# Kernel optimization log

Measured on AMD Instinct MI355X. Metric: run time of the kernel, lower is better.

## Reference

```python
import jax, jax.numpy as jnp
import numpy as np

GS, GL, LS, LL, NA = 8, 8, 16, 8, 12
ALPHA = 0.5


def _rgb_to_lab(img):
    # img: (B,3,H,W) in [0,1]. Standard sRGB -> CIELab (kornia convention).
    lin = jnp.where(img > 0.04045, ((img + 0.055) / 1.055) ** 2.4, img / 12.92)
    r, g, b = lin[:, 0], lin[:, 1], lin[:, 2]
    x = 0.412453 * r + 0.357580 * g + 0.180423 * b
    y = 0.212671 * r + 0.715160 * g + 0.072169 * b
    z = 0.019334 * r + 0.119193 * g + 0.950227 * b
    xn, yn, zn = x / 0.950456, y, z / 1.088754
    f = lambda t: jnp.where(t > 0.008856, jnp.cbrt(t), 7.787 * t + 4.0 / 29.0)
    fx, fy, fz = f(xn), f(yn), f(zn)
    L = 116.0 * fy - 16.0
    a = 500.0 * (fx - fy)
    bb = 200.0 * (fy - fz)
    return L, a, bb


def _bilateral_slice(grid, img, guide):
    # grid: (B,12,s,s,l); img: (B,3,H,W); guide: (B,H,W) in [0,1]
    B, C, s, _, l = grid.shape
    _, _, H, W = img.shape
    g5 = jnp.transpose(grid, (0, 4, 2, 3, 1))  # (B, D=l, Hg=s, Wg=s, C)
    # align_corners=True coordinates, border padding == clamp
    fx = jnp.linspace(0.0, s - 1.0, W)                    # (W,)
    fy = jnp.linspace(0.0, s - 1.0, H)                    # (H,)
    fz = jnp.clip(guide * (l - 1.0), 0.0, l - 1.0)        # (B,H,W)
    x0 = jnp.floor(fx).astype(jnp.int32); x1 = jnp.minimum(x0 + 1, s - 1)
    y0 = jnp.floor(fy).astype(jnp.int32); y1 = jnp.minimum(y0 + 1, s - 1)
    z0 = jnp.floor(fz).astype(jnp.int32); z1 = jnp.minimum(z0 + 1, l - 1)
    wx = (fx - x0)[None, None, :, None]
    wy = (fy - y0)[None, :, None, None]
    wz = (fz - z0)[..., None]
    bi = jnp.arange(B)[:, None, None]
    yi0, yi1 = y0[None, :, None], y1[None, :, None]
    xi0, xi1 = x0[None, None, :], x1[None, None, :]

    def gat(zi, yi, xi):
        return g5[bi, zi, yi, xi]  # (B,H,W,C)

    def bilin(zi):
        c00 = gat(zi, yi0, xi0) * (1 - wx) + gat(zi, yi0, xi1) * wx
        c10 = gat(zi, yi1, xi0) * (1 - wx) + gat(zi, yi1, xi1) * wx
        return c00 * (1 - wy) + c10 * wy

    coeffs = bilin(z0) * (1 - wz) + bilin(z1) * wz       # (B,H,W,12)
    A = coeffs[..., :9].reshape(B, H, W, 3, 3)
    bvec = coeffs[..., 9:]
    img_hwc = jnp.transpose(img, (0, 2, 3, 1))           # (B,H,W,3)
    out = jnp.einsum('bhwck,bhwk->bhwc', A, img_hwc) + bvec
    return jnp.transpose(jnp.clip(out, 0.0, 1.0), (0, 3, 1, 2))


def setup_inputs() -> dict:
    key = jax.random.key(0)
    ks = jax.random.split(key, 16)
    B, H, W = 4, 896, 896
    n_h = n_w = 64
    inp = {
        'R_spatial': jax.random.normal(ks[0], (B, 256, n_h, n_w), jnp.float32),
        'F_sem': jax.random.normal(ks[1], (B, n_h * n_w, 384), jnp.float32),
        'img': jax.random.uniform(ks[2], (B, 3, H, W), jnp.float32),
        'n_h': n_h,
        'n_w': n_w,
    }
    sc = 0.02
    identity = np.array([1., 0., 0., 0., 1., 0., 0., 0., 1., 0., 0., 0.], np.float32)
    inp['dino_proj_w'] = jax.random.normal(ks[3], (128, 384), jnp.float32) * sc
    inp['dino_proj_b'] = jnp.zeros((128,), jnp.float32)
    inp['fusion_w'] = jax.random.normal(ks[4], (256, 384), jnp.float32) * sc
    inp['fusion_b'] = jnp.zeros((256,), jnp.float32)
    inp['g1_w'] = jax.random.normal(ks[5], (256, 256), jnp.float32) * sc
    inp['g1_b'] = jnp.zeros((256,), jnp.float32)
    inp['g2_w'] = jax.random.normal(ks[6], (NA * GS * GS * GL, 256), jnp.float32) * sc
    inp['g2_b'] = jnp.asarray(np.repeat(identity, GS * GS * GL))  # identity init
    inp['local_w'] = jax.random.normal(ks[7], (NA * LL, 256), jnp.float32) * sc
    inp['local_b'] = jnp.asarray(np.repeat(identity, LL))
    inp['guide_w1'] = jax.random.normal(ks[8], (64, 384), jnp.float32) * sc
    inp['guide_b1'] = jnp.zeros((64,), jnp.float32)
    inp['guide_w2'] = jax.random.normal(ks[9], (1, 64), jnp.float32) * sc
    inp['guide_b2'] = jnp.zeros((1,), jnp.float32)
    return inp


def reference(R_spatial, F_sem, img, n_h, n_w,
              dino_proj_w, dino_proj_b, fusion_w, fusion_b,
              g1_w, g1_b, g2_w, g2_b, local_w, local_b,
              guide_w1, guide_b1, guide_w2, guide_b2):
    B, _, H, W = img.shape
    # ---- GridNet ----
    F_sp = jnp.transpose(F_sem, (0, 2, 1)).reshape(B, 384, n_h, n_w)
    proj = jnp.einsum('bchw,oc->bohw', F_sp, dino_proj_w) + dino_proj_b[None, :, None, None]
    fused_in = jnp.concatenate([R_spatial, proj], axis=1)
    fused = jnp.einsum('bchw,oc->bohw', fused_in, fusion_w) + fusion_b[None, :, None, None]
    f_gap = fused.mean(axis=(-2, -1))                       # (B,256)
    h = jax.nn.relu(f_gap @ g1_w.T + g1_b)
    G_global = (h @ g2_w.T + g2_b).reshape(B, NA, GS, GS, GL)
    kh, kw = n_h // LS, n_w // LS
    pooled = fused.reshape(B, 256, LS, kh, LS, kw).mean(axis=(3, 5))
    lflat = jnp.einsum('bchw,oc->bohw', pooled, local_w) + local_b[None, :, None, None]
    G_local = jnp.transpose(lflat.reshape(B, NA, LL, LS, LS), (0, 1, 3, 4, 2))
    # ---- SemanticGuide ----
    L, a, bb = _rgb_to_lab(img)
    g_chroma = jnp.clip((0.5 * L + 0.25 * jnp.abs(a) + 0.25 * jnp.abs(bb)) / 114.0, 0.0, 1.0)
    hsem = jax.nn.relu(jnp.einsum('bnd,hd->bnh', F_sem, guide_w1) + guide_b1)
    g_sem_patch = jax.nn.sigmoid(jnp.einsum('bnh,oh->bno', hsem, guide_w2) + guide_b2)
    g_sem_patch = g_sem_patch.reshape(B, n_h, n_w, 1).transpose(0, 3, 1, 2)
    g_sem = jax.image.resize(g_sem_patch, (B, 1, H, W), 'bilinear')[:, 0]
    g = ALPHA * g_chroma + (1.0 - ALPHA) * g_sem
    # ---- slice + apply ----
    I_global = _bilateral_slice(G_global, img, g)
    I_local = _bilateral_slice(G_local, img, g)
    return I_global, I_local, G_global, G_local, g
```

## Files before the change

### kernel.cpp

```cpp
#include <hip/hip_runtime.h>
#include <math.h>

#define HWPIX 802816
#define OUT_IL 9633792
#define OUT_GG 19267584
#define OUT_GL 19292160
#define OUT_G  19390464

#define WS_WT4  0
#define WS_BC   163840
#define WS_POOL 164096
#define WS_H    426240
#define WS_GSEM 427264
#define WS_RG   443648
#define WS_RL   468224
#define WS_W1T  566528

__device__ __forceinline__ float fast_exp2(float x) {
  return __builtin_amdgcn_exp2f(x);
}
__device__ __forceinline__ float fast_log2(float x) {
  return __builtin_amdgcn_logf(x);
}
__device__ __forceinline__ float srgb_lin(float v) {
  float p = fast_exp2(2.4f * fast_log2((v + 0.055f) * (1.0f / 1.055f)));
  return v > 0.04045f ? p : v * (1.0f / 12.92f);
}
__device__ __forceinline__ float labf(float t) {
  float c = fast_exp2((1.0f / 3.0f) * fast_log2(t));
  return t > 0.008856f ? c : 7.787f * t + (4.0f / 29.0f);
}

__global__ __launch_bounds__(256) void k_prep(
    const float* __restrict__ fus_w, const float* __restrict__ fus_b,
    const float* __restrict__ dino_w, const float* __restrict__ dino_b,
    const float* __restrict__ gw1, float* __restrict__ Wt4,
    float* __restrict__ bc, float* __restrict__ w1T) {
  if (blockIdx.x == 641) {
    int t = threadIdx.x;
    for (int it = 0; it < 96; ++it) {
      int idx = it * 256 + t;
      int h = idx & 63;
      int k = idx >> 6;
      w1T[((k >> 2) * 64 + h) * 4 + (k & 3)] = gw1[h * 384 + k];
    }
    return;
  }
  if (blockIdx.x == 640) {
    int o = threadIdx.x;
    float acc = fus_b[o];
    for (int m = 0; m < 128; ++m) acc += fus_w[o * 384 + 256 + m] * dino_b[m];
    bc[o] = acc;
    return;
  }
  int idx = blockIdx.x * 256 + threadIdx.x;
  int o = idx / 640;
  int k = idx - o * 640;
  float val;
  if (k < 256) {
    val = fus_w[o * 384 + k];
  } else {
    int d = k - 256;
    float acc = 0.0f;
    for (int m = 0; m < 128; ++m)
      acc += fus_w[o * 384 + 256 + m] * dino_w[m * 384 + d];
    val = acc;
  }
  Wt4[((k >> 2) * 256 + o) * 4 + (k & 3)] = val;
}

__global__ __launch_bounds__(1024) void k_fused_pool(
    const float* __restrict__ R, const float* __restrict__ F,
    const float* __restrict__ Wt4, const float* __restrict__ bc,
    float* __restrict__ pooled) {
  int blk = blockIdx.x;
  int b = blk >> 6;
  int i = (blk >> 2) & 15;
  int jg = blk & 3;
  int t = threadIdx.x;
  int cell = t >> 8;
  int c = t & 255;
  __shared__ float s[4 * 640];
  {
    const float* rb = R + (((b * 256 + c) * 64 + i * 4) * 64) + (jg * 4 + cell) * 4;
    float p = 0.0f;
#pragma unroll
    for (int di = 0; di < 4; ++di) {
      float4 v = *(const float4*)(rb + di * 64);
      p += v.x + v.y + v.z + v.w;
    }
    s[cell * 640 + c] = p;
  }
  {
    float a0 = 0.0f, a1 = 0.0f;
    const float* fb = F + (size_t)(b * 4096 + (i * 4) * 64 + (jg * 4 + cell) * 4) * 384;
#pragma unroll
    for (int pix = 0; pix < 16; ++pix) {
      const float* fr = fb + (size_t)((pix >> 2) * 64 + (pix & 3)) * 384;
      a0 += fr[c];
      if (c < 128) a1 += fr[256 + c];
    }
    s[cell * 640 + 256 + c] = a0;
    if (c < 128) s[cell * 640 + 512 + c] = a1;
  }
  __syncthreads();
  float acc = 0.0f;
  const float4* w4 = (const float4*)Wt4;
  const float4* s4 = (const float4*)(s + cell * 640);
#pragma unroll 8
  for (int kk = 0; kk < 160; ++kk) {
    float4 wv = w4[kk * 256 + c];
    float4 sv = s4[kk];
    acc += wv.x * sv.x + wv.y * sv.y + wv.z * sv.z + wv.w * sv.w;
  }
  __syncthreads();
  s[cell * 256 + c] = acc;
  __syncthreads();
  if (t < 256) {
    float bco = bc[t];
    float4 v;
    v.x = s[0 * 256 + t] * (1.0f / 16.0f) + bco;
    v.y = s[1 * 256 + t] * (1.0f / 16.0f) + bco;
    v.z = s[2 * 256 + t] * (1.0f / 16.0f) + bco;
    v.w = s[3 * 256 + t] * (1.0f / 16.0f) + bco;
    *(float4*)(pooled + ((size_t)(b * 256 + t) * 256) + i * 16 + jg * 4) = v;
  }
}

__global__ __launch_bounds__(1024) void k_gap(
    const float* __restrict__ pooled, const float* __restrict__ g1_w,
    const float* __restrict__ g1_b, float* __restrict__ hout) {
  int b = blockIdx.x;
  int t = threadIdx.x;
  int o = t & 255;
  int q = t >> 8;
  __shared__ float f[256];
  __shared__ float part[4][256];
  {
    const float4* pr4 = (const float4*)(pooled + (size_t)(b * 256 + o) * 256 + q * 64);
    float s = 0.0f;
#pragma unroll
    for (int i = 0; i < 16; ++i) {
      float4 v = pr4[i];
      s += v.x + v.y + v.z + v.w;
    }
    part[q][o] = s;
  }
  __syncthreads();
  if (t < 256)
    f[t] = (part[0][t] + part[1][t] + part[2][t] + part[3][t]) * (1.0f / 256.0f);
  __syncthreads();
  {
    const float4* wr = (const float4*)(g1_w + o * 256 + q * 64);
    const float4* fq = (const float4*)(f + q * 64);
    float acc = 0.0f;
#pragma unroll
    for (int i = 0; i < 16; ++i) {
      float4 w = wr[i];
      float4 fv = fq[i];
      acc += w.x * fv.x + w.y * fv.y + w.z * fv.z + w.w * fv.w;
    }
    part[q][o] = acc;
  }
  __syncthreads();
  if (t < 256) {
    float a = part[0][t] + part[1][t] + part[2][t] + part[3][t] + g1_b[t];
    hout[b * 256 + t] = fmaxf(a, 0.0f);
  }
}

__global__ __launch_bounds__(256) void k_gglobal(
    const float* __restrict__ h, const float* __restrict__ g2_w,
    const float* __restrict__ g2_b, float* __restrict__ out3,
    float* __restrict__ rg) {
  int b = blockIdx.x / 24;
  int o = (blockIdx.x % 24) * 256 + threadIdx.x;
  __shared__ float hl[256];
  hl[threadIdx.x] = h[b * 256 + threadIdx.x];
  __syncthreads();
  float acc = g2_b[o];
  const float* wr = g2_w + o * 256;
  for (int k = 0; k < 256; ++k) acc += wr[k] * hl[k];
  out3[b * 6144 + o] = acc;
  int n = o >> 9, y = (o >> 6) & 7, x = (o >> 3) & 7, z = o & 7;
  rg[b * 6144 + ((y * 8 + x) * 8 + z) * 12 + n] = acc;
}

__global__ __launch_bounds__(256) void k_glocal(
    const float* __restrict__ pooled, const float* __restrict__ lw,
    const float* __restrict__ lb, float* __restrict__ out4,
    float* __restrict__ rl) {
  int idx = blockIdx.x * 256 + threadIdx.x;
  int b = idx / 24576;
  int r = idx - b * 24576;
  int o = r >> 8;
  int cell = r & 255;
  float acc = lb[o];
  const float* wr = lw + o * 256;
  const float* pr = pooled + b * 65536 + cell;
  for (int c = 0; c < 256; ++c) acc += wr[c] * pr[c * 256];
  int n = o >> 3, l = o & 7;
  out4[((b * 12 + n) * 256 + cell) * 8 + l] = acc;
  rl[b * 24576 + (cell * 8 + l) * 12 + n] = acc;
}

__global__ __launch_bounds__(256) void k_guide(
    const float* __restrict__ F, const float* __restrict__ w1T,
    const float* __restrict__ b1, const float* __restrict__ w2,
    const float* __restrict__ b2, float* __restrict__ gsem) {
  int t = threadIdx.x;
  int wave = t >> 6;
  int lane = t & 63;
  int pb = blockIdx.x * 16;
  __shared__ float4 sF[16 * 96];
  const float4* Fb = (const float4*)(F + (size_t)pb * 384);
#pragma unroll
  for (int r = 0; r < 6; ++r) sF[r * 256 + t] = Fb[r * 256 + t];
  __syncthreads();
  float accp[4] = {0.0f, 0.0f, 0.0f, 0.0f};
  const float4* w4 = (const float4*)w1T;
  int prow = wave * 4;
  for (int c = 0; c < 48; ++c) {
    float4 wa = w4[(c * 2 + 0) * 64 + lane];
    float4 wb = w4[(c * 2 + 1) * 64 + lane];
#pragma unroll
    for (int p = 0; p < 4; ++p) {
      float4 va = sF[(prow + p) * 96 + c * 2 + 0];
      float4 vb = sF[(prow + p) * 96 + c * 2 + 1];
      accp[p] += va.x * wa.x + va.y * wa.y + va.z * wa.z + va.w * wa.w +
                 vb.x * wb.x + vb.y * wb.y + vb.z * wb.z + vb.w * wb.w;
    }
  }
  float hb = b1[lane];
  float wl = w2[lane];
  float b2v = b2[0];
  float res = 0.0f;
#pragma unroll
  for (int p = 0; p < 4; ++p) {
    float v = fmaxf(accp[p] + hb, 0.0f) * wl;
#pragma unroll
    for (int m = 32; m >= 1; m >>= 1) v += __shfl_xor(v, m, 64);
    if (lane == p) res = v;
  }
  if (lane < 4) gsem[pb + prow + lane] = 1.0f / (1.0f + expf(-(res + b2v)));
}

template <int SDIM>
__device__ __forceinline__ void slice_lds(
    const float* __restrict__ sg, int w, int z0, int z1, float wz,
    float r, float g, float bl, float& o0, float& o1, float& o2) {
  constexpr float sc = (float)(SDIM - 1) * (1.0f / 895.0f);
  float fxs = (float)w * sc;
  int x0 = (int)fxs;
  if (x0 > SDIM - 1) x0 = SDIM - 1;
  int x1 = x0 < SDIM - 1 ? x0 + 1 : SDIM - 1;
  float wx = fxs - (float)x0;
  float wz0 = 1.0f - wz;
  float w00 = (1.0f - wx) * wz0;
  float w01 = (1.0f - wx) * wz;
  float w10 = wx * wz0;
  float w11 = wx * wz;
  const float4* p00 = (const float4*)(sg + (x0 * 8 + z0) * 12);
  const float4* p01 = (const float4*)(sg + (x0 * 8 + z1) * 12);
  const float4* p10 = (const float4*)(sg + (x1 * 8 + z0) * 12);
  const float4* p11 = (const float4*)(sg + (x1 * 8 + z1) * 12);
  float a[12];
#pragma unroll
  for (int c = 0; c < 3; ++c) {
    float4 v00 = p00[c], v01 = p01[c], v10 = p10[c], v11 = p11[c];
    a[4 * c + 0] = w00 * v00.x + w01 * v01.x + w10 * v10.x + w11 * v11.x;
    a[4 * c + 1] = w00 * v00.y + w01 * v01.y + w10 * v10.y + w11 * v11.y;
    a[4 * c + 2] = w00 * v00.z + w01 * v01.z + w10 * v10.z + w11 * v11.z;
    a[4 * c + 3] = w00 * v00.w + w01 * v01.w + w10 * v10.w + w11 * v11.w;
  }
  o0 = fminf(fmaxf(a[0] * r + a[1] * g + a[2] * bl + a[9], 0.0f), 1.0f);
  o1 = fminf(fmaxf(a[3] * r + a[4] * g + a[5] * bl + a[10], 0.0f), 1.0f);
  o2 = fminf(fmaxf(a[6] * r + a[7] * g + a[8] * bl + a[11], 0.0f), 1.0f);
}

__global__ __launch_bounds__(448) void k_pixel(
    const float* __restrict__ img, const float* __restrict__ gsem,
    const float* __restrict__ rg, const float* __restrict__ rl,
    float* __restrict__ out) {
  int blk = blockIdx.x;
  int b = blk / 896;
  int h = blk - b * 896;
  int t = threadIdx.x;
  __shared__ float sgr[64];
  __shared__ float sG[768];
  __shared__ float sL[1536];

  float sy = fminf(fmaxf((h + 0.5f) * (1.0f / 14.0f) - 0.5f, 0.0f), 63.0f);
  int y0s = (int)sy;
  int y1s = y0s < 63 ? y0s + 1 : 63;
  float wys = sy - (float)y0s;
  float fyg = (float)h * (7.0f / 895.0f);
  int y0g = (int)fyg;
  if (y0g > 7) y0g = 7;
  int y1g = y0g < 7 ? y0g + 1 : 7;
  float wyg = fyg - (float)y0g;
  float fyl = (float)h * (15.0f / 895.0f);
  int y0l = (int)fyl;
  if (y0l > 15) y0l = 15;
  int y1l = y0l < 15 ? y0l + 1 : 15;
  float wyl = fyl - (float)y0l;

  if (t < 64) {
    const float* gb = gsem + b * 4096;
    sgr[t] = gb[y0s * 64 + t] * (1.0f - wys) + gb[y1s * 64 + t] * wys;
  }
  {
    const float* g0 = rg + b * 6144 + y0g * 768;
    const float* g1 = rg + b * 6144 + y1g * 768;
    for (int i = t; i < 768; i += 448)
      sG[i] = g0[i] * (1.0f - wyg) + g1[i] * wyg;
    const float* l0 = rl + b * 24576 + y0l * 1536;
    const float* l1 = rl + b * 24576 + y1l * 1536;
    for (int i = t; i < 1536; i += 448)
      sL[i] = l0[i] * (1.0f - wyl) + l1[i] * wyl;
  }
  __syncthreads();

#pragma unroll
  for (int ip = 0; ip < 2; ++ip) {
    int w = ip * 448 + t;
    int hw = h * 896 + w;
    float r = img[(b * 3 + 0) * HWPIX + hw];
    float g = img[(b * 3 + 1) * HWPIX + hw];
    float bl = img[(b * 3 + 2) * HWPIX + hw];
    float lr = srgb_lin(r), lg = srgb_lin(g), lb2 = srgb_lin(bl);
    float X = 0.412453f * lr + 0.357580f * lg + 0.180423f * lb2;
    float Y = 0.212671f * lr + 0.715160f * lg + 0.072169f * lb2;
    float Z = 0.019334f * lr + 0.119193f * lg + 0.950227f * lb2;
    float fx_ = labf(X * (1.0f / 0.950456f));
    float fy_ = labf(Y);
    float fz_ = labf(Z * (1.0f / 1.088754f));
    float gch = 0.50877193f * fy_ - 0.070175439f +
                1.0964912f * fabsf(fx_ - fy_) + 0.43859649f * fabsf(fy_ - fz_);
    gch = fminf(fmaxf(gch, 0.0f), 1.0f);
    float sx = fminf(fmaxf((w + 0.5f) * (1.0f / 14.0f) - 0.5f, 0.0f), 63.0f);
    int x0s = (int)sx;
    int x1s = x0s < 63 ? x0s + 1 : 63;
    float wxs = sx - (float)x0s;
    float gs = sgr[x0s] * (1.0f - wxs) + sgr[x1s] * wxs;
    float gg = 0.5f * gch + 0.5f * gs;
    __builtin_nontemporal_store(gg, &out[OUT_G + b * HWPIX + hw]);
    float fzc = fminf(fmaxf(gg * 7.0f, 0.0f), 7.0f);
    int z0 = (int)fzc;
    if (z0 > 7) z0 = 7;
    int z1 = z0 < 7 ? z0 + 1 : 7;
    float wz = fzc - (float)z0;
    float o0, o1, o2;
    slice_lds<8>(sG, w, z0, z1, wz, r, g, bl, o0, o1, o2);
    __builtin_nontemporal_store(o0, &out[(b * 3 + 0) * HWPIX + hw]);
    __builtin_nontemporal_store(o1, &out[(b * 3 + 1) * HWPIX + hw]);
    __builtin_nontemporal_store(o2, &out[(b * 3 + 2) * HWPIX + hw]);
    slice_lds<16>(sL, w, z0, z1, wz, r, g, bl, o0, o1, o2);
    __builtin_nontemporal_store(o0, &out[OUT_IL + (b * 3 + 0) * HWPIX + hw]);
    __builtin_nontemporal_store(o1, &out[OUT_IL + (b * 3 + 1) * HWPIX + hw]);
    __builtin_nontemporal_store(o2, &out[OUT_IL + (b * 3 + 2) * HWPIX + hw]);
  }
}

extern "C" void kernel_launch(void* const* d_in, const int* in_sizes, int n_in,
                              void* d_out, int out_size, void* d_ws,
                              size_t ws_size, hipStream_t stream) {
  const float* R = (const float*)d_in[0];
  const float* F = (const float*)d_in[1];
  const float* img = (const float*)d_in[2];
  const float* dino_w = (const float*)d_in[5];
  const float* dino_b = (const float*)d_in[6];
  const float* fus_w = (const float*)d_in[7];
  const float* fus_b = (const float*)d_in[8];
  const float* g1_w = (const float*)d_in[9];
  const float* g1_b = (const float*)d_in[10];
  const float* g2_w = (const float*)d_in[11];
  const float* g2_b = (const float*)d_in[12];
  const float* lw = (const float*)d_in[13];
  const float* lb = (const float*)d_in[14];
  const float* gw1 = (const float*)d_in[15];
  const float* gb1 = (const float*)d_in[16];
  const float* gw2 = (const float*)d_in[17];
  const float* gb2 = (const float*)d_in[18];
  float* out = (float*)d_out;
  float* ws = (float*)d_ws;

  float* Wt4 = ws + WS_WT4;
  float* bc = ws + WS_BC;
  float* pooled = ws + WS_POOL;
  float* hbuf = ws + WS_H;
  float* gsem = ws + WS_GSEM;
  float* rg = ws + WS_RG;
  float* rl = ws + WS_RL;
  float* w1T = ws + WS_W1T;

  k_prep<<<642, 256, 0, stream>>>(fus_w, fus_b, dino_w, dino_b, gw1, Wt4, bc, w1T);
  k_guide<<<1024, 256, 0, stream>>>(F, w1T, gb1, gw2, gb2, gsem);
  k_fused_pool<<<256, 1024, 0, stream>>>(R, F, Wt4, bc, pooled);
  k_gap<<<4, 1024, 0, stream>>>(pooled, g1_w, g1_b, hbuf);
  k_gglobal<<<96, 256, 0, stream>>>(hbuf, g2_w, g2_b, out + OUT_GG, rg);
  k_glocal<<<384, 256, 0, stream>>>(pooled, lw, lb, out + OUT_GL, rl);
  k_pixel<<<3584, 448, 0, stream>>>(img, gsem, rg, rl, out);
}
```

Measured before the change: 324.1 us.

## Fuse local grid projection into pooling kernel and split-K the global grid matvec

The local-grid 1x1 projection moves from its own kernel into the tail of k_fused_pool, using the pooled values still held in shared memory and a transposed copy of the local weights built in k_prep. This removes one kernel launch and the strided re-read of the pooled buffer. k_gglobal now splits its 256-long dot product across four thread groups with float4 loads and a shared-memory reduction. The fused tail runs a serial 256-step loop per thread on part of the block, which lengthens the pooling kernel.

```diff
diff --git a/kernel.cpp b/kernel.cpp
--- a/kernel.cpp
+++ b/kernel.cpp
@@ -15,6 +15,7 @@
 #define WS_RG   443648
 #define WS_RL   468224
 #define WS_W1T  566528
+#define WS_LWT  591104
 
 __device__ __forceinline__ float fast_exp2(float x) {
   return __builtin_amdgcn_exp2f(x);
@@ -34,8 +35,19 @@
 __global__ __launch_bounds__(256) void k_prep(
     const float* __restrict__ fus_w, const float* __restrict__ fus_b,
     const float* __restrict__ dino_w, const float* __restrict__ dino_b,
-    const float* __restrict__ gw1, float* __restrict__ Wt4,
-    float* __restrict__ bc, float* __restrict__ w1T) {
+    const float* __restrict__ gw1, const float* __restrict__ lw,
+    float* __restrict__ Wt4, float* __restrict__ bc, float* __restrict__ w1T,
+    float* __restrict__ lwT) {
+  if (blockIdx.x == 642) {
+    int t = threadIdx.x;
+    for (int it = 0; it < 96; ++it) {
+      int idx = it * 256 + t;
+      int o = idx >> 8;
+      int c = idx & 255;
+      lwT[c * 96 + o] = lw[o * 256 + c];
+    }
+    return;
+  }
   if (blockIdx.x == 641) {
     int t = threadIdx.x;
     for (int it = 0; it < 96; ++it) {
@@ -72,7 +84,9 @@
 __global__ __launch_bounds__(1024) void k_fused_pool(
     const float* __restrict__ R, const float* __restrict__ F,
     const float* __restrict__ Wt4, const float* __restrict__ bc,
-    float* __restrict__ pooled) {
+    const float* __restrict__ lwT, const float* __restrict__ lb,
+    float* __restrict__ pooled, float* __restrict__ out4,
+    float* __restrict__ rl) {
   int blk = blockIdx.x;
   int b = blk >> 6;
   int i = (blk >> 2) & 15;
@@ -124,6 +138,20 @@
     v.z = s[2 * 256 + t] * (1.0f / 16.0f) + bco;
     v.w = s[3 * 256 + t] * (1.0f / 16.0f) + bco;
     *(float4*)(pooled + ((size_t)(b * 256 + t) * 256) + i * 16 + jg * 4) = v;
+  } else if (t < 640) {
+    int idx = t - 256;
+    int cl = idx / 96;
+    int o = idx - cl * 96;
+    const float* sc_ = s + cl * 256;
+    float acc2 = lb[o];
+    for (int cc = 0; cc < 256; ++cc) {
+      float pv = sc_[cc] * (1.0f / 16.0f) + bc[cc];
+      acc2 += lwT[cc * 96 + o] * pv;
+    }
+    int cellg = i * 16 + jg * 4 + cl;
+    int n = o >> 3, l = o & 7;
+    out4[((b * 12 + n) * 256 + cellg) * 8 + l] = acc2;
+    rl[b * 24576 + (cellg * 8 + l) * 12 + n] = acc2;
   }
 }
 
@@ -169,39 +197,39 @@
   }
 }
 
-__global__ __launch_bounds__(256) void k_gglobal(
+__global__ __launch_bounds__(1024) void k_gglobal(
     const float* __restrict__ h, const float* __restrict__ g2_w,
     const float* __restrict__ g2_b, float* __restrict__ out3,
     float* __restrict__ rg) {
   int b = blockIdx.x / 24;
-  int o = (blockIdx.x % 24) * 256 + threadIdx.x;
+  int og = (blockIdx.x % 24) * 256;
+  int t = threadIdx.x;
+  int ol = t & 255;
+  int q = t >> 8;
   __shared__ float hl[256];
-  hl[threadIdx.x] = h[b * 256 + threadIdx.x];
-  __syncthreads();
-  float acc = g2_b[o];
-  const float* wr = g2_w + o * 256;
-  for (int k = 0; k < 256; ++k) acc += wr[k] * hl[k];
-  out3[b * 6144 + o] = acc;
-  int n = o >> 9, y = (o >> 6) & 7, x = (o >> 3) & 7, z = o & 7;
-  rg[b * 6144 + ((y * 8 + x) * 8 + z) * 12 + n] = acc;
-}
-
-__global__ __launch_bounds__(256) void k_glocal(
-    const float* __restrict__ pooled, const float* __restrict__ lw,
-    const float* __restrict__ lb, float* __restrict__ out4,
-    float* __restrict__ rl) {
-  int idx = blockIdx.x * 256 + threadIdx.x;
-  int b = idx / 24576;
-  int r = idx - b * 24576;
-  int o = r >> 8;
-  int cell = r & 255;
-  float acc = lb[o];
-  const float* wr = lw + o * 256;
-  const float* pr = pooled + b * 65536 + cell;
-  for (int c = 0; c < 256; ++c) acc += wr[c] * pr[c * 256];
-  int n = o >> 3, l = o & 7;
-  out4[((b * 12 + n) * 256 + cell) * 8 + l] = acc;
-  rl[b * 24576 + (cell * 8 + l) * 12 + n] = acc;
+  __shared__ float part[4][256];
+  if (t < 256) hl[t] = h[b * 256 + t];
+  __syncthreads();
+  {
+    const float4* wr = (const float4*)(g2_w + (size_t)(og + ol) * 256 + q * 64);
+    const float4* hq = (const float4*)(hl + q * 64);
+    float acc = 0.0f;
+#pragma unroll
+    for (int i = 0; i < 16; ++i) {
+      float4 w = wr[i];
+      float4 hv = hq[i];
+      acc += w.x * hv.x + w.y * hv.y + w.z * hv.z + w.w * hv.w;
+    }
+    part[q][ol] = acc;
+  }
+  __syncthreads();
+  if (t < 256) {
+    int o = og + t;
+    float a = part[0][t] + part[1][t] + part[2][t] + part[3][t] + g2_b[o];
+    out3[b * 6144 + o] = a;
+    int n = o >> 9, y = (o >> 6) & 7, x = (o >> 3) & 7, z = o & 7;
+    rg[b * 6144 + ((y * 8 + x) * 8 + z) * 12 + n] = a;
+  }
 }
 
 __global__ __launch_bounds__(256) void k_guide(
@@ -393,12 +421,14 @@
   float* rg = ws + WS_RG;
   float* rl = ws + WS_RL;
   float* w1T = ws + WS_W1T;
-
-  k_prep<<<642, 256, 0, stream>>>(fus_w, fus_b, dino_w, dino_b, gw1, Wt4, bc, w1T);
+  float* lwT = ws + WS_LWT;
+
+  k_prep<<<643, 256, 0, stream>>>(fus_w, fus_b, dino_w, dino_b, gw1, lw,
+                                  Wt4, bc, w1T, lwT);
   k_guide<<<1024, 256, 0, stream>>>(F, w1T, gb1, gw2, gb2, gsem);
-  k_fused_pool<<<256, 1024, 0, stream>>>(R, F, Wt4, bc, pooled);
+  k_fused_pool<<<256, 1024, 0, stream>>>(R, F, Wt4, bc, lwT, lb,
+                                         pooled, out + OUT_GL, rl);
   k_gap<<<4, 1024, 0, stream>>>(pooled, g1_w, g1_b, hbuf);
-  k_gglobal<<<96, 256, 0, stream>>>(hbuf, g2_w, g2_b, out + OUT_GG, rg);
-  k_glocal<<<384, 256, 0, stream>>>(pooled, lw, lb, out + OUT_GL, rl);
+  k_gglobal<<<96, 1024, 0, stream>>>(hbuf, g2_w, g2_b, out + OUT_GG, rg);
   k_pixel<<<3584, 448, 0, stream>>>(img, gsem, rg, rl, out);
 }
```

After: 318.1 us. No clear change (-1.9%).
